# Optimization experiments

Measured on AMD Instinct MI355X. Metric: run time of the kernel, lower is better.

Reference implementation:

```python
import jax, jax.numpy as jnp
import numpy as np

H = 1024      # controller hidden size
M = 4096      # memory rows (must equal WORD per original code's buffer shapes)
WORD = 4096   # word size
R = 4         # read heads
NW = 2        # write heads
MODES = 1 + 2 * NW
EPS = 1e-3


def _lin(x, W, b):
    return x @ W.T + b


def _allocation(usage):
    # usage: [1, M] -> allocation weighting via ascending usage sort (DNC)
    u = EPS + (1.0 - EPS) * usage
    order = jnp.argsort(u, axis=1)                       # ascending (least used first)
    sorted_u = jnp.take_along_axis(u, order, axis=1)
    prod = jnp.cumprod(sorted_u, axis=1)
    excl = jnp.concatenate([jnp.ones((1, 1), u.dtype), prod[:, :-1]], axis=1)
    sorted_alloc = (1.0 - sorted_u) * excl
    return jnp.zeros_like(u).at[0, order[0]].set(sorted_alloc[0])


def _dnc_forward(x, memory, prev_read_weights, prev_write_weights, prev_link,
                 prev_precedence, prev_usage,
                 W_wv, b_wv, W_ev, b_ev, W_fg, b_fg, W_ag, b_ag, W_wg, b_wg,
                 W_rm, b_rm, W_wk, b_wk, W_ws, b_ws, W_rk, b_rk, W_rs, b_rs):
    # ---- read_inputs ----
    write_vector = _lin(x, W_wv, b_wv).reshape(NW, WORD)
    erase_vector = jax.nn.sigmoid(_lin(x, W_ev, b_ev)).reshape(NW, WORD)
    free_gate = jax.nn.sigmoid(_lin(x, W_fg, b_fg))          # [1,R]
    allocation_gate = jax.nn.sigmoid(_lin(x, W_ag, b_ag))    # [1,NW]
    write_gate = jax.nn.sigmoid(_lin(x, W_wg, b_wg))         # [1,NW]
    read_mode = jax.nn.sigmoid(_lin(x, W_rm, b_rm)).reshape(R, MODES)
    write_keys = jax.nn.sigmoid(_lin(x, W_wk, b_wk)).reshape(NW, WORD)
    write_strengths = _lin(x, W_ws, b_ws)                    # [1,NW]
    read_keys = _lin(x, W_rk, b_rk).reshape(R, WORD)
    read_strengths = _lin(x, W_rs, b_rs)                     # [1,R]

    # ---- usage ----
    ww_term = 1.0 - jnp.prod(prev_write_weights, axis=1)                   # [1,M]
    usage = prev_usage + (1.0 - prev_usage) * ww_term
    phi = 1.0 - jnp.prod(free_gate[..., None] * prev_read_weights, axis=1)
    usage = usage * phi

    # ---- write weights (cosine content + sequential allocation per head) ----
    dot = jnp.einsum('wd,bmd->bwm', write_keys, memory)                    # [1,NW,M]
    mem_norms = jnp.sqrt(jnp.sum(memory * memory, axis=2))                 # [1,M]
    key_norms = jnp.sqrt(jnp.sum(write_keys * write_keys, axis=1))         # [NW]
    similarity = dot / (key_norms[None, :, None] * mem_norms[:, None, :] + EPS)

    write_gates = (allocation_gate * write_gate)[..., None]                # [1,NW,1]
    ww_rows = []
    for i in range(NW):  # small fixed head loop (sequential usage dependency)
        beta = 1.0 + jax.nn.softplus(write_strengths[0, i])
        cw = jax.nn.softmax(similarity[0, i] * beta)                       # [M]
        a = _allocation(usage)                                             # [1,M]
        usage = usage + (1.0 - usage) * write_gates[:, i, :] * a
        ww_rows.append(write_gate[0, i] * (allocation_gate[0, i] * a[0]
                       + (1.0 - allocation_gate[0, i]) * cw))
    write_weights = jnp.stack(ww_rows)[None]                               # [1,NW,M]

    # ---- erase and write ----
    weighted_resets = write_weights[..., None] * erase_vector[None, :, None, :]
    reset_gate = jnp.prod(1.0 - weighted_resets, axis=1)                   # [1,M,WORD]
    new_memory = memory * reset_gate + jnp.einsum('bwm,wd->bmd', write_weights, write_vector)

    # ---- temporal linkage ----
    wi = write_weights[..., None]          # [1,NW,M,1]
    wj = write_weights[:, :, None, :]      # [1,NW,1,M]
    pj = prev_precedence[:, :, None, :]    # [1,NW,1,M]
    link = (1.0 - wi - wj) * prev_link + wi * pj
    link = link * (1.0 - jnp.eye(M, dtype=link.dtype))
    write_sum = jnp.sum(write_weights, axis=2, keepdims=True)
    precedence = (1.0 - write_sum) * prev_precedence + write_weights

    # ---- read weights ----
    rdot = jnp.einsum('rd,bmd->brm', read_keys, new_memory)
    new_mem_norms = jnp.sqrt(jnp.sum(new_memory * new_memory, axis=2))
    rkey_norms = jnp.sqrt(jnp.sum(read_keys * read_keys, axis=1))
    rsim = rdot / (rkey_norms[None, :, None] * new_mem_norms[:, None, :])  # note: no eps here (as in source)
    content_weights = jax.nn.softmax(rsim * read_strengths[0][None, :, None], axis=-1)

    expanded = jnp.broadcast_to(prev_read_weights[:, None], (1, NW, R, M))  # stack((rw,rw)) with NW=2
    fwd_w = jnp.einsum('bwrm,bwnm->brwn', expanded, link)   # rw @ link^T, permuted -> [1,R,NW,M]
    bwd_w = jnp.einsum('bwrm,bwmn->brwn', expanded, link)   # rw @ link,   permuted -> [1,R,NW,M]
    rm = read_mode[None]                                    # [1,R,MODES]
    backward_mode = rm[:, :, :NW]
    forward_mode = rm[:, :, NW:2 * NW]
    content_mode = rm[:, :, 2 * NW:]                        # [1,R,1]
    read_weights = (jnp.einsum('brw,brwm->brm', backward_mode, bwd_w)
                    + jnp.einsum('brw,brwm->brm', forward_mode, fwd_w)
                    + content_mode * content_weights)
    read_words = jnp.einsum('brm,bmd->brd', read_weights, new_memory)      # [1,R,WORD]
    return read_words, new_memory, read_weights, write_weights, link, precedence, usage


def setup_inputs() -> dict:
    key = jax.random.key(0)
    ks = jax.random.split(key, 32)
    rn = lambda i, s: jax.random.normal(ks[i], s, dtype=jnp.float32)
    ru = lambda i, s: jax.random.uniform(ks[i], s, dtype=jnp.float32)
    w = lambda i, s: rn(i, s) * 0.02
    return {
        'x': rn(0, (1, H)),
        'memory': rn(1, (1, M, WORD)),
        'prev_read_weights': ru(2, (1, R, M)),
        'prev_write_weights': ru(3, (1, NW, M)),
        'prev_link': ru(4, (1, NW, M, M)),
        'prev_precedence': ru(5, (1, NW, M)),
        'prev_usage': ru(6, (1, M)),
        'W_wv': w(7, (NW * WORD, H)), 'b_wv': jnp.zeros((NW * WORD,), jnp.float32),
        'W_ev': w(8, (NW * WORD, H)), 'b_ev': jnp.zeros((NW * WORD,), jnp.float32),
        'W_fg': w(9, (R, H)), 'b_fg': jnp.zeros((R,), jnp.float32),
        'W_ag': w(10, (NW, H)), 'b_ag': jnp.zeros((NW,), jnp.float32),
        'W_wg': w(11, (NW, H)), 'b_wg': jnp.zeros((NW,), jnp.float32),
        'W_rm': w(12, (R * MODES, H)), 'b_rm': jnp.zeros((R * MODES,), jnp.float32),
        'W_wk': w(13, (NW * WORD, H)), 'b_wk': jnp.zeros((NW * WORD,), jnp.float32),
        'W_ws': w(14, (NW, H)), 'b_ws': jnp.zeros((NW,), jnp.float32),
        'W_rk': w(15, (R * WORD, H)), 'b_rk': jnp.zeros((R * WORD,), jnp.float32),
        'W_rs': w(16, (R, H)), 'b_rs': jnp.zeros((R,), jnp.float32),
    }


def reference(x, memory, prev_read_weights, prev_write_weights, prev_link,
              prev_precedence, prev_usage,
              W_wv, b_wv, W_ev, b_ev, W_fg, b_fg, W_ag, b_ag, W_wg, b_wg,
              W_rm, b_rm, W_wk, b_wk, W_ws, b_ws, W_rk, b_rk, W_rs, b_rs):
    return _dnc_forward(x, memory, prev_read_weights, prev_write_weights, prev_link,
                        prev_precedence, prev_usage,
                        W_wv, b_wv, W_ev, b_ev, W_fg, b_fg, W_ag, b_ag, W_wg, b_wg,
                        W_rm, b_rm, W_wk, b_wk, W_ws, b_ws, W_rk, b_rk, W_rs, b_rs)
```

## Files before the change

### kernel.cpp

```cpp
#include <hip/hip_runtime.h>
#include <math.h>

#define HD 1024
#define MD 4096
#define WD 4096
#define RD 4
#define NWD 2
#define MODESD 5
#define EPSF 0.001f

#define O_WORDS 0
#define O_NM    16384
#define O_RW    16793600
#define O_WW    16809984
#define O_LINK  16818176
#define O_PREC  50372608
#define O_USAGE 50380800

#define WS_WV   0
#define WS_EV   8192
#define WS_WK   16384
#define WS_RK   24576
#define WS_FG   40960
#define WS_AG   40976
#define WS_WG   40992
#define WS_RM   41008
#define WS_WSTR 41040
#define WS_RS   41056
#define WS_KN   41072
#define WS_RKN  41088
#define WS_UPRE 41104
#define WS_SIM  45200
#define WS_RDOT 53392
#define WS_NMN  69776
#define WS_CONT 73872
#define WS_FWD  90256
#define WS_CW   123024
#define WS_UU   131216
#define WS_LU   135312
#define WS_S0   139408
#define WS_S1   143504
#define WS_WWSUM 147600
#define WS_BWD  147604
#define WS_ZERO_START WS_S0
#define WS_ZERO_COUNT (4096 + 4096 + 4 + 32768)

__device__ __forceinline__ float waveReduceSum(float v) {
#pragma unroll
  for (int o = 32; o; o >>= 1) v += __shfl_down(v, o, 64);
  return v;
}

__global__ void gemv_kernel(const float* __restrict__ W, const float* __restrict__ b,
                            const float* __restrict__ x, float* __restrict__ out,
                            int rows, int act) {
  __shared__ float4 xs[HD / 4];
  int t = threadIdx.x;
  const float4* x4 = (const float4*)x;
  xs[t] = x4[t];
  __syncthreads();
  int wave = t >> 6, lane = t & 63;
  int row = blockIdx.x * 4 + wave;
  if (row >= rows) return;
  const float4* W4 = (const float4*)(W + (size_t)row * HD);
  float acc = 0.f;
#pragma unroll
  for (int i = 0; i < 4; ++i) {
    float4 w = W4[i * 64 + lane];
    float4 xv = xs[i * 64 + lane];
    acc += w.x * xv.x + w.y * xv.y + w.z * xv.z + w.w * xv.w;
  }
  acc = waveReduceSum(acc);
  if (lane == 0) {
    float v = acc + b[row];
    if (act) v = 1.f / (1.f + expf(-v));
    out[row] = v;
  }
}

__global__ void small_gemv_kernel(const float* __restrict__ x,
                                  const float* __restrict__ Wfg, const float* __restrict__ bfg,
                                  const float* __restrict__ Wag, const float* __restrict__ bag,
                                  const float* __restrict__ Wwg, const float* __restrict__ bwg,
                                  const float* __restrict__ Wrm, const float* __restrict__ brm,
                                  const float* __restrict__ Wws, const float* __restrict__ bws,
                                  const float* __restrict__ Wrs, const float* __restrict__ brs,
                                  float* __restrict__ ws) {
  int blk = blockIdx.x;
  const float* W; const float* b; float* out; int row; int act;
  if (blk < 4)       { W = Wfg; b = bfg; out = ws + WS_FG;   row = blk;       act = 1; }
  else if (blk < 6)  { W = Wag; b = bag; out = ws + WS_AG;   row = blk - 4;   act = 1; }
  else if (blk < 8)  { W = Wwg; b = bwg; out = ws + WS_WG;   row = blk - 6;   act = 1; }
  else if (blk < 28) { W = Wrm; b = brm; out = ws + WS_RM;   row = blk - 8;   act = 1; }
  else if (blk < 30) { W = Wws; b = bws; out = ws + WS_WSTR; row = blk - 28;  act = 0; }
  else               { W = Wrs; b = brs; out = ws + WS_RS;   row = blk - 30;  act = 0; }
  int t = threadIdx.x;
  const float4* W4 = (const float4*)(W + (size_t)row * HD);
  const float4* x4 = (const float4*)x;
  float4 w = W4[t], xv = x4[t];
  float acc = w.x * xv.x + w.y * xv.y + w.z * xv.z + w.w * xv.w;
  acc = waveReduceSum(acc);
  __shared__ float sh[4];
  int wave = t >> 6, lane = t & 63;
  if (lane == 0) sh[wave] = acc;
  __syncthreads();
  if (t == 0) {
    float v = sh[0] + sh[1] + sh[2] + sh[3] + b[row];
    if (act) v = 1.f / (1.f + expf(-v));
    out[row] = v;
  }
}

__global__ void norms_kernel(const float* __restrict__ wk, const float* __restrict__ rk,
                             float* __restrict__ kn, float* __restrict__ rkn) {
  int v = blockIdx.x;
  const float* p = (v < 2) ? (wk + v * WD) : (rk + (v - 2) * WD);
  float s = 0.f;
  for (int d = threadIdx.x; d < WD; d += 256) { float t = p[d]; s += t * t; }
  s = waveReduceSum(s);
  __shared__ float sh[4];
  int wave = threadIdx.x >> 6, lane = threadIdx.x & 63;
  if (lane == 0) sh[wave] = s;
  __syncthreads();
  if (threadIdx.x == 0) {
    float r = sqrtf(sh[0] + sh[1] + sh[2] + sh[3]);
    if (v < 2) kn[v] = r; else rkn[v - 2] = r;
  }
}

__global__ void usage_kernel(const float* __restrict__ pusage, const float* __restrict__ pww,
                             const float* __restrict__ prw, const float* __restrict__ fg,
                             float* __restrict__ upre, float* __restrict__ uu,
                             float* __restrict__ lu) {
  int m = blockIdx.x * 256 + threadIdx.x;
  float pw = 1.f;
#pragma unroll
  for (int w = 0; w < NWD; ++w) pw *= pww[w * MD + m];
  float pu = pusage[m];
  float u = pu + (1.f - pu) * (1.f - pw);
  float pr = 1.f;
#pragma unroll
  for (int r = 0; r < RD; ++r) pr *= fg[r] * prw[r * MD + m];
  float up = u * (1.f - pr);
  upre[m] = up;
  float v = EPSF + (1.f - EPSF) * up;
  uu[m] = v;
  lu[m] = logf(v);
}

__global__ void sim_kernel(const float* __restrict__ mem, const float* __restrict__ wk,
                           const float* __restrict__ kn, float* __restrict__ sim) {
  int m = blockIdx.x;
  int t = threadIdx.x;
  const float4* row = (const float4*)(mem + (size_t)m * WD);
  const float4* k0 = (const float4*)wk;
  const float4* k1 = (const float4*)(wk + WD);
  float d0 = 0, d1 = 0, s = 0;
  for (int i = t; i < WD / 4; i += 256) {
    float4 v = row[i], a = k0[i], b = k1[i];
    d0 += v.x * a.x + v.y * a.y + v.z * a.z + v.w * a.w;
    d1 += v.x * b.x + v.y * b.y + v.z * b.z + v.w * b.w;
    s  += v.x * v.x + v.y * v.y + v.z * v.z + v.w * v.w;
  }
  d0 = waveReduceSum(d0); d1 = waveReduceSum(d1); s = waveReduceSum(s);
  __shared__ float sh[3][4];
  int wave = t >> 6, lane = t & 63;
  if (lane == 0) { sh[0][wave] = d0; sh[1][wave] = d1; sh[2][wave] = s; }
  __syncthreads();
  if (t == 0) {
    float D0 = sh[0][0] + sh[0][1] + sh[0][2] + sh[0][3];
    float D1 = sh[1][0] + sh[1][1] + sh[1][2] + sh[1][3];
    float S  = sh[2][0] + sh[2][1] + sh[2][2] + sh[2][3];
    float mn = sqrtf(S);
    sim[0 * MD + m] = D0 / (kn[0] * mn + EPSF);
    sim[1 * MD + m] = D1 / (kn[1] * mn + EPSF);
  }
}

__global__ void cw_kernel(const float* __restrict__ sim, const float* __restrict__ wstr,
                          float* __restrict__ cw) {
  int h = blockIdx.x;
  int t = threadIdx.x;
  __shared__ float vals[MD];
  __shared__ float red[256];
  float beta = 1.f + log1pf(expf(wstr[h]));
  float mx = -3.4e38f;
  for (int m = t; m < MD; m += 256) {
    float v = sim[h * MD + m] * beta;
    vals[m] = v; mx = fmaxf(mx, v);
  }
  red[t] = mx; __syncthreads();
  for (int s = 128; s; s >>= 1) { if (t < s) red[t] = fmaxf(red[t], red[t + s]); __syncthreads(); }
  mx = red[0]; __syncthreads();
  float sm = 0.f;
  for (int m = t; m < MD; m += 256) { float e = expf(vals[m] - mx); vals[m] = e; sm += e; }
  red[t] = sm; __syncthreads();
  for (int s = 128; s; s >>= 1) { if (t < s) red[t] += red[t + s]; __syncthreads(); }
  float inv = 1.f / red[0];
  for (int m = t; m < MD; m += 256) cw[h * MD + m] = vals[m] * inv;
}

__global__ void alloc_partial_kernel(const float* __restrict__ uu, const float* __restrict__ lu,
                                     float* __restrict__ S) {
  __shared__ float4 us[64], ls[64];
  int t = threadIdx.x;
  int j0 = blockIdx.y * 256;
  if (t < 64) {
    us[t] = ((const float4*)(uu + j0))[t];
    ls[t] = ((const float4*)(lu + j0))[t];
  }
  __syncthreads();
  int i = blockIdx.x * 256 + t;
  float ui = uu[i];
  float s = 0.f;
#pragma unroll 4
  for (int c = 0; c < 64; ++c) {
    float4 u4 = us[c], l4 = ls[c];
    int jb = j0 + c * 4;
    s += ((u4.x < ui) || (u4.x == ui && (jb + 0) < i)) ? l4.x : 0.f;
    s += ((u4.y < ui) || (u4.y == ui && (jb + 1) < i)) ? l4.y : 0.f;
    s += ((u4.z < ui) || (u4.z == ui && (jb + 2) < i)) ? l4.z : 0.f;
    s += ((u4.w < ui) || (u4.w == ui && (jb + 3) < i)) ? l4.w : 0.f;
  }
  atomicAdd(&S[i], s);
}

__global__ void update0_kernel(const float* __restrict__ S0, const float* __restrict__ cw,
                               const float* __restrict__ ag, const float* __restrict__ wg,
                               const float* __restrict__ upre, float* __restrict__ uu,
                               float* __restrict__ lu, float* __restrict__ u1,
                               float* __restrict__ out_ww, float* __restrict__ wwsum) {
  int m = blockIdx.x * 256 + threadIdx.x;
  float agv = ag[0], wgv = wg[0];
  float uum = uu[m];
  float a = (1.f - uum) * expf(S0[m]);
  float w = wgv * (agv * a + (1.f - agv) * cw[m]);
  out_ww[m] = w;
  float up = upre[m];
  float un = up + (1.f - up) * (agv * wgv) * a;
  u1[m] = un;
  float v = EPSF + (1.f - EPSF) * un;
  uu[m] = v;
  lu[m] = logf(v);
  float p = waveReduceSum(w);
  if ((threadIdx.x & 63) == 0) atomicAdd(&wwsum[0], p);
}

__global__ void update1_kernel(const float* __restrict__ S1, const float* __restrict__ cw,
                               const float* __restrict__ ag, const float* __restrict__ wg,
                               const float* __restrict__ u1, const float* __restrict__ uu,
                               float* __restrict__ out_ww, float* __restrict__ out_usage,
                               float* __restrict__ wwsum) {
  int m = blockIdx.x * 256 + threadIdx.x;
  float agv = ag[1], wgv = wg[1];
  float uum = uu[m];
  float a = (1.f - uum) * expf(S1[m]);
  float w = wgv * (agv * a + (1.f - agv) * cw[MD + m]);
  out_ww[MD + m] = w;
  float un = u1[m];
  out_usage[m] = un + (1.f - un) * (agv * wgv) * a;
  float p = waveReduceSum(w);
  if ((threadIdx.x & 63) == 0) atomicAdd(&wwsum[1], p);
}

__global__ void prec_kernel(const float* __restrict__ ww, const float* __restrict__ wwsum,
                            const float* __restrict__ pprec, float* __restrict__ out_prec) {
  int m = blockIdx.x * 256 + threadIdx.x;
  float s0 = wwsum[0], s1 = wwsum[1];
  out_prec[m] = (1.f - s0) * pprec[m] + ww[m];
  out_prec[MD + m] = (1.f - s1) * pprec[MD + m] + ww[MD + m];
}

__global__ void newmem_kernel(const float* __restrict__ mem, const float* __restrict__ ww,
                              const float* __restrict__ ev, const float* __restrict__ wvv,
                              const float* __restrict__ rk, float* __restrict__ nm_out,
                              float* __restrict__ rdot, float* __restrict__ nmn) {
  int m = blockIdx.x;
  int t = threadIdx.x;
  float w0 = ww[m], w1 = ww[MD + m];
  const float4* row = (const float4*)(mem + (size_t)m * WD);
  const float4* e0 = (const float4*)ev;
  const float4* e1 = (const float4*)(ev + WD);
  const float4* v0 = (const float4*)wvv;
  const float4* v1 = (const float4*)(wvv + WD);
  const float4* k0 = (const float4*)rk;
  const float4* k1 = (const float4*)(rk + WD);
  const float4* k2 = (const float4*)(rk + 2 * WD);
  const float4* k3 = (const float4*)(rk + 3 * WD);
  float4* outp = (float4*)(nm_out + (size_t)m * WD);
  float r0 = 0, r1 = 0, r2 = 0, r3 = 0, s2 = 0;
  for (int i = t; i < WD / 4; i += 256) {
    float4 mv = row[i], ea = e0[i], eb = e1[i], va = v0[i], vb = v1[i];
    float4 o;
    o.x = mv.x * (1.f - w0 * ea.x) * (1.f - w1 * eb.x) + w0 * va.x + w1 * vb.x;
    o.y = mv.y * (1.f - w0 * ea.y) * (1.f - w1 * eb.y) + w0 * va.y + w1 * vb.y;
    o.z = mv.z * (1.f - w0 * ea.z) * (1.f - w1 * eb.z) + w0 * va.z + w1 * vb.z;
    o.w = mv.w * (1.f - w0 * ea.w) * (1.f - w1 * eb.w) + w0 * va.w + w1 * vb.w;
    outp[i] = o;
    float4 a = k0[i]; r0 += o.x * a.x + o.y * a.y + o.z * a.z + o.w * a.w;
    float4 b = k1[i]; r1 += o.x * b.x + o.y * b.y + o.z * b.z + o.w * b.w;
    float4 c = k2[i]; r2 += o.x * c.x + o.y * c.y + o.z * c.z + o.w * c.w;
    float4 d = k3[i]; r3 += o.x * d.x + o.y * d.y + o.z * d.z + o.w * d.w;
    s2 += o.x * o.x + o.y * o.y + o.z * o.z + o.w * o.w;
  }
  r0 = waveReduceSum(r0); r1 = waveReduceSum(r1); r2 = waveReduceSum(r2);
  r3 = waveReduceSum(r3); s2 = waveReduceSum(s2);
  __shared__ float sh[5][4];
  int wave = t >> 6, lane = t & 63;
  if (lane == 0) { sh[0][wave] = r0; sh[1][wave] = r1; sh[2][wave] = r2; sh[3][wave] = r3; sh[4][wave] = s2; }
  __syncthreads();
  if (t == 0) {
    rdot[0 * MD + m] = sh[0][0] + sh[0][1] + sh[0][2] + sh[0][3];
    rdot[1 * MD + m] = sh[1][0] + sh[1][1] + sh[1][2] + sh[1][3];
    rdot[2 * MD + m] = sh[2][0] + sh[2][1] + sh[2][2] + sh[2][3];
    rdot[3 * MD + m] = sh[3][0] + sh[3][1] + sh[3][2] + sh[3][3];
    nmn[m] = sqrtf(sh[4][0] + sh[4][1] + sh[4][2] + sh[4][3]);
  }
}

__global__ void content_kernel(const float* __restrict__ rdot, const float* __restrict__ nmn,
                               const float* __restrict__ rkn, const float* __restrict__ rs,
                               float* __restrict__ cont) {
  int r = blockIdx.x;
  int t = threadIdx.x;
  __shared__ float vals[MD];
  __shared__ float red[256];
  float strength = rs[r], kn = rkn[r];
  float mx = -3.4e38f;
  for (int m = t; m < MD; m += 256) {
    float v = rdot[r * MD + m] / (kn * nmn[m]) * strength;
    vals[m] = v; mx = fmaxf(mx, v);
  }
  red[t] = mx; __syncthreads();
  for (int s = 128; s; s >>= 1) { if (t < s) red[t] = fmaxf(red[t], red[t + s]); __syncthreads(); }
  mx = red[0]; __syncthreads();
  float sm = 0.f;
  for (int m = t; m < MD; m += 256) { float e = expf(vals[m] - mx); vals[m] = e; sm += e; }
  red[t] = sm; __syncthreads();
  for (int s = 128; s; s >>= 1) { if (t < s) red[t] += red[t + s]; __syncthreads(); }
  float inv = 1.f / red[0];
  for (int m = t; m < MD; m += 256) cont[r * MD + m] = vals[m] * inv;
}

__global__ void link_kernel(const float* __restrict__ plink, const float* __restrict__ ww,
                            const float* __restrict__ pprec, const float* __restrict__ prw,
                            float* __restrict__ link_out, float* __restrict__ fwd) {
  int i = blockIdx.x;
  int w = blockIdx.y;
  int t = threadIdx.x;
  float wwi = ww[w * MD + i];
  const float4* pl = (const float4*)(plink + ((size_t)w * MD + i) * MD);
  const float4* wj = (const float4*)(ww + w * MD);
  const float4* pj = (const float4*)(pprec + w * MD);
  const float4* p0 = (const float4*)prw;
  const float4* p1 = (const float4*)(prw + MD);
  const float4* p2 = (const float4*)(prw + 2 * MD);
  const float4* p3 = (const float4*)(prw + 3 * MD);
  float4* lo = (float4*)(link_out + ((size_t)w * MD + i) * MD);
  float f0 = 0, f1 = 0, f2 = 0, f3 = 0;
  for (int c = t; c < MD / 4; c += 256) {
    float4 L = pl[c], WJ = wj[c], PJ = pj[c];
    float4 o;
    o.x = (1.f - wwi - WJ.x) * L.x + wwi * PJ.x;
    o.y = (1.f - wwi - WJ.y) * L.y + wwi * PJ.y;
    o.z = (1.f - wwi - WJ.z) * L.z + wwi * PJ.z;
    o.w = (1.f - wwi - WJ.w) * L.w + wwi * PJ.w;
    int j0 = c * 4;
    if ((unsigned)(i - j0) < 4u) ((float*)&o)[i - j0] = 0.f;
    lo[c] = o;
    float4 a = p0[c]; f0 += o.x * a.x + o.y * a.y + o.z * a.z + o.w * a.w;
    float4 b = p1[c]; f1 += o.x * b.x + o.y * b.y + o.z * b.z + o.w * b.w;
    float4 cc = p2[c]; f2 += o.x * cc.x + o.y * cc.y + o.z * cc.z + o.w * cc.w;
    float4 d = p3[c]; f3 += o.x * d.x + o.y * d.y + o.z * d.z + o.w * d.w;
  }
  f0 = waveReduceSum(f0); f1 = waveReduceSum(f1);
  f2 = waveReduceSum(f2); f3 = waveReduceSum(f3);
  __shared__ float sh[4][4];
  int wave = t >> 6, lane = t & 63;
  if (lane == 0) { sh[0][wave] = f0; sh[1][wave] = f1; sh[2][wave] = f2; sh[3][wave] = f3; }
  __syncthreads();
  if (t == 0) {
    fwd[(0 * NWD + w) * MD + i] = sh[0][0] + sh[0][1] + sh[0][2] + sh[0][3];
    fwd[(1 * NWD + w) * MD + i] = sh[1][0] + sh[1][1] + sh[1][2] + sh[1][3];
    fwd[(2 * NWD + w) * MD + i] = sh[2][0] + sh[2][1] + sh[2][2] + sh[2][3];
    fwd[(3 * NWD + w) * MD + i] = sh[3][0] + sh[3][1] + sh[3][2] + sh[3][3];
  }
}

__global__ void bwd_kernel(const float* __restrict__ link, const float* __restrict__ prw,
                           float* __restrict__ bwd) {
  int mc = blockIdx.x, jt = blockIdx.y, w = blockIdx.z;
  int j = jt * 256 + threadIdx.x;
  const float* base = link + (size_t)w * MD * MD;
  float a0 = 0, a1 = 0, a2 = 0, a3 = 0;
  int m0 = mc * 256;
  for (int m = m0; m < m0 + 256; ++m) {
    float lv = base[(size_t)m * MD + j];
    a0 += prw[m] * lv;
    a1 += prw[MD + m] * lv;
    a2 += prw[2 * MD + m] * lv;
    a3 += prw[3 * MD + m] * lv;
  }
  atomicAdd(&bwd[(0 * NWD + w) * MD + j], a0);
  atomicAdd(&bwd[(1 * NWD + w) * MD + j], a1);
  atomicAdd(&bwd[(2 * NWD + w) * MD + j], a2);
  atomicAdd(&bwd[(3 * NWD + w) * MD + j], a3);
}

__global__ void rw_kernel(const float* __restrict__ fwd, const float* __restrict__ bwd,
                          const float* __restrict__ cont, const float* __restrict__ rm,
                          float* __restrict__ out_rw) {
  int idx = blockIdx.x * 256 + threadIdx.x;
  int r = idx >> 12;
  int m = idx & (MD - 1);
  float v = rm[r * MODESD + 4] * cont[idx];
#pragma unroll
  for (int w = 0; w < NWD; ++w) {
    v += rm[r * MODESD + w] * bwd[(r * NWD + w) * MD + m];
    v += rm[r * MODESD + NWD + w] * fwd[(r * NWD + w) * MD + m];
  }
  out_rw[idx] = v;
}

__global__ void rwords_kernel(const float* __restrict__ rw, const float* __restrict__ nm,
                              float* __restrict__ out_words) {
  int mc = blockIdx.x;
  int d = blockIdx.y * 256 + threadIdx.x;
  float a0 = 0, a1 = 0, a2 = 0, a3 = 0;
  int m0 = mc * 256;
  for (int m = m0; m < m0 + 256; ++m) {
    float v = nm[(size_t)m * WD + d];
    a0 += rw[m] * v;
    a1 += rw[MD + m] * v;
    a2 += rw[2 * MD + m] * v;
    a3 += rw[3 * MD + m] * v;
  }
  atomicAdd(&out_words[d], a0);
  atomicAdd(&out_words[WD + d], a1);
  atomicAdd(&out_words[2 * WD + d], a2);
  atomicAdd(&out_words[3 * WD + d], a3);
}

extern "C" void kernel_launch(void* const* d_in, const int* in_sizes, int n_in,
                              void* d_out, int out_size, void* d_ws, size_t ws_size,
                              hipStream_t stream) {
  (void)in_sizes; (void)n_in; (void)out_size; (void)ws_size;
  const float* x      = (const float*)d_in[0];
  const float* memory = (const float*)d_in[1];
  const float* prw    = (const float*)d_in[2];
  const float* pww    = (const float*)d_in[3];
  const float* plink  = (const float*)d_in[4];
  const float* pprec  = (const float*)d_in[5];
  const float* pusage = (const float*)d_in[6];
  float* ws  = (float*)d_ws;
  float* out = (float*)d_out;

  hipMemsetAsync(ws + WS_ZERO_START, 0, WS_ZERO_COUNT * sizeof(float), stream);
  hipMemsetAsync(out + O_WORDS, 0, 16384 * sizeof(float), stream);

  gemv_kernel<<<2048, 256, 0, stream>>>((const float*)d_in[7],  (const float*)d_in[8],  x, ws + WS_WV, 8192, 0);
  gemv_kernel<<<2048, 256, 0, stream>>>((const float*)d_in[9],  (const float*)d_in[10], x, ws + WS_EV, 8192, 1);
  gemv_kernel<<<2048, 256, 0, stream>>>((const float*)d_in[19], (const float*)d_in[20], x, ws + WS_WK, 8192, 1);
  gemv_kernel<<<4096, 256, 0, stream>>>((const float*)d_in[23], (const float*)d_in[24], x, ws + WS_RK, 16384, 0);
  small_gemv_kernel<<<34, 256, 0, stream>>>(x,
      (const float*)d_in[11], (const float*)d_in[12],
      (const float*)d_in[13], (const float*)d_in[14],
      (const float*)d_in[15], (const float*)d_in[16],
      (const float*)d_in[17], (const float*)d_in[18],
      (const float*)d_in[21], (const float*)d_in[22],
      (const float*)d_in[25], (const float*)d_in[26],
      ws);

  norms_kernel<<<6, 256, 0, stream>>>(ws + WS_WK, ws + WS_RK, ws + WS_KN, ws + WS_RKN);
  usage_kernel<<<16, 256, 0, stream>>>(pusage, pww, prw, ws + WS_FG, ws + WS_UPRE, ws + WS_UU, ws + WS_LU);
  sim_kernel<<<4096, 256, 0, stream>>>(memory, ws + WS_WK, ws + WS_KN, ws + WS_SIM);
  cw_kernel<<<2, 256, 0, stream>>>(ws + WS_SIM, ws + WS_WSTR, ws + WS_CW);

  alloc_partial_kernel<<<dim3(16, 16), 256, 0, stream>>>(ws + WS_UU, ws + WS_LU, ws + WS_S0);
  update0_kernel<<<16, 256, 0, stream>>>(ws + WS_S0, ws + WS_CW, ws + WS_AG, ws + WS_WG,
                                         ws + WS_UPRE, ws + WS_UU, ws + WS_LU, ws + WS_UPRE,
                                         out + O_WW, ws + WS_WWSUM);
  alloc_partial_kernel<<<dim3(16, 16), 256, 0, stream>>>(ws + WS_UU, ws + WS_LU, ws + WS_S1);
  update1_kernel<<<16, 256, 0, stream>>>(ws + WS_S1, ws + WS_CW, ws + WS_AG, ws + WS_WG,
                                         ws + WS_UPRE, ws + WS_UU, out + O_WW, out + O_USAGE,
                                         ws + WS_WWSUM);
  prec_kernel<<<16, 256, 0, stream>>>(out + O_WW, ws + WS_WWSUM, pprec, out + O_PREC);

  newmem_kernel<<<4096, 256, 0, stream>>>(memory, out + O_WW, ws + WS_EV, ws + WS_WV,
                                          ws + WS_RK, out + O_NM, ws + WS_RDOT, ws + WS_NMN);
  content_kernel<<<4, 256, 0, stream>>>(ws + WS_RDOT, ws + WS_NMN, ws + WS_RKN, ws + WS_RS, ws + WS_CONT);
  link_kernel<<<dim3(MD, NWD), 256, 0, stream>>>(plink, out + O_WW, pprec, prw,
                                                 out + O_LINK, ws + WS_FWD);
  bwd_kernel<<<dim3(16, 16, 2), 256, 0, stream>>>(out + O_LINK, prw, ws + WS_BWD);
  rw_kernel<<<64, 256, 0, stream>>>(ws + WS_FWD, ws + WS_BWD, ws + WS_CONT, ws + WS_RM, out + O_RW);
  rwords_kernel<<<dim3(16, 16), 256, 0, stream>>>(out + O_RW, out + O_NM, out + O_WORDS);
}
```

Before: 684.7 us.

## Fuse GEMVs, alloc chain with grid barrier, and link forward/backward passes

Merges all controller GEMVs into one launch with nontemporal weight loads, folds the key norms into the sim and content kernels, and collapses the usage/allocation/update/precedence sequence into one 64-block kernel synchronised by a software grid barrier. The link update is tiled so that a single pass over the two 64MB link matrices computes the new link (written with nontemporal stores) together with the forward and backward products, instead of rereading the link in a separate backward kernel. The grid barrier assumes all 64 blocks are resident at once, and atomics now accumulate forward and backward partials.

```diff
diff --git a/kernel.cpp b/kernel.cpp
--- a/kernel.cpp
+++ b/kernel.cpp
@@ -27,23 +27,34 @@
 #define WS_RM   41008
 #define WS_WSTR 41040
 #define WS_RS   41056
-#define WS_KN   41072
-#define WS_RKN  41088
 #define WS_UPRE 41104
 #define WS_SIM  45200
 #define WS_RDOT 53392
 #define WS_NMN  69776
 #define WS_CONT 73872
-#define WS_FWD  90256
 #define WS_CW   123024
 #define WS_UU   131216
 #define WS_LU   135312
-#define WS_S0   139408
-#define WS_S1   143504
+#define WS_S0    139408
+#define WS_S1    143504
 #define WS_WWSUM 147600
-#define WS_BWD  147604
+#define WS_BAR   147604
+#define WS_FWD   147620
+#define WS_BWD   180388
 #define WS_ZERO_START WS_S0
-#define WS_ZERO_COUNT (4096 + 4096 + 4 + 32768)
+#define WS_ZERO_COUNT (213156 - 139408)
+
+typedef float floatx4 __attribute__((ext_vector_type(4)));
+
+__device__ __forceinline__ float4 ntload4(const float4* p) {
+  floatx4 t = __builtin_nontemporal_load((const floatx4*)p);
+  float4 r; r.x = t.x; r.y = t.y; r.z = t.z; r.w = t.w;
+  return r;
+}
+__device__ __forceinline__ void ntstore4(float4* p, float4 v) {
+  floatx4 t; t.x = v.x; t.y = v.y; t.z = v.z; t.w = v.w;
+  __builtin_nontemporal_store(t, (floatx4*)p);
+}
 
 __device__ __forceinline__ float waveReduceSum(float v) {
 #pragma unroll
@@ -51,129 +62,84 @@
   return v;
 }
 
-__global__ void gemv_kernel(const float* __restrict__ W, const float* __restrict__ b,
-                            const float* __restrict__ x, float* __restrict__ out,
-                            int rows, int act) {
+__global__ void __launch_bounds__(256) gemv_all_kernel(
+    const float* __restrict__ x,
+    const float* __restrict__ Wwv, const float* __restrict__ bwv,
+    const float* __restrict__ Wev, const float* __restrict__ bev,
+    const float* __restrict__ Wwk, const float* __restrict__ bwk,
+    const float* __restrict__ Wrk, const float* __restrict__ brk,
+    const float* __restrict__ Wfg, const float* __restrict__ bfg,
+    const float* __restrict__ Wag, const float* __restrict__ bag,
+    const float* __restrict__ Wwg, const float* __restrict__ bwg,
+    const float* __restrict__ Wrm, const float* __restrict__ brm,
+    const float* __restrict__ Wws, const float* __restrict__ bws,
+    const float* __restrict__ Wrs, const float* __restrict__ brs,
+    float* __restrict__ ws) {
   __shared__ float4 xs[HD / 4];
   int t = threadIdx.x;
-  const float4* x4 = (const float4*)x;
-  xs[t] = x4[t];
+  xs[t] = ((const float4*)x)[t];
   __syncthreads();
   int wave = t >> 6, lane = t & 63;
   int row = blockIdx.x * 4 + wave;
-  if (row >= rows) return;
-  const float4* W4 = (const float4*)(W + (size_t)row * HD);
+  if (row >= 40994) return;
+  const float* W; const float* b; float* out; int r; int act;
+  if (row < 8192)       { W = Wwv; b = bwv; out = ws + WS_WV;   r = row;         act = 0; }
+  else if (row < 16384) { W = Wev; b = bev; out = ws + WS_EV;   r = row - 8192;  act = 1; }
+  else if (row < 24576) { W = Wwk; b = bwk; out = ws + WS_WK;   r = row - 16384; act = 1; }
+  else if (row < 40960) { W = Wrk; b = brk; out = ws + WS_RK;   r = row - 24576; act = 0; }
+  else if (row < 40964) { W = Wfg; b = bfg; out = ws + WS_FG;   r = row - 40960; act = 1; }
+  else if (row < 40966) { W = Wag; b = bag; out = ws + WS_AG;   r = row - 40964; act = 1; }
+  else if (row < 40968) { W = Wwg; b = bwg; out = ws + WS_WG;   r = row - 40966; act = 1; }
+  else if (row < 40988) { W = Wrm; b = brm; out = ws + WS_RM;   r = row - 40968; act = 1; }
+  else if (row < 40990) { W = Wws; b = bws; out = ws + WS_WSTR; r = row - 40988; act = 0; }
+  else                  { W = Wrs; b = brs; out = ws + WS_RS;   r = row - 40990; act = 0; }
+  const float4* W4 = (const float4*)(W + (size_t)r * HD);
   float acc = 0.f;
 #pragma unroll
   for (int i = 0; i < 4; ++i) {
-    float4 w = W4[i * 64 + lane];
+    float4 w = ntload4(W4 + i * 64 + lane);
     float4 xv = xs[i * 64 + lane];
     acc += w.x * xv.x + w.y * xv.y + w.z * xv.z + w.w * xv.w;
   }
   acc = waveReduceSum(acc);
   if (lane == 0) {
-    float v = acc + b[row];
+    float v = acc + b[r];
     if (act) v = 1.f / (1.f + expf(-v));
-    out[row] = v;
-  }
-}
-
-__global__ void small_gemv_kernel(const float* __restrict__ x,
-                                  const float* __restrict__ Wfg, const float* __restrict__ bfg,
-                                  const float* __restrict__ Wag, const float* __restrict__ bag,
-                                  const float* __restrict__ Wwg, const float* __restrict__ bwg,
-                                  const float* __restrict__ Wrm, const float* __restrict__ brm,
-                                  const float* __restrict__ Wws, const float* __restrict__ bws,
-                                  const float* __restrict__ Wrs, const float* __restrict__ brs,
-                                  float* __restrict__ ws) {
-  int blk = blockIdx.x;
-  const float* W; const float* b; float* out; int row; int act;
-  if (blk < 4)       { W = Wfg; b = bfg; out = ws + WS_FG;   row = blk;       act = 1; }
-  else if (blk < 6)  { W = Wag; b = bag; out = ws + WS_AG;   row = blk - 4;   act = 1; }
-  else if (blk < 8)  { W = Wwg; b = bwg; out = ws + WS_WG;   row = blk - 6;   act = 1; }
-  else if (blk < 28) { W = Wrm; b = brm; out = ws + WS_RM;   row = blk - 8;   act = 1; }
-  else if (blk < 30) { W = Wws; b = bws; out = ws + WS_WSTR; row = blk - 28;  act = 0; }
-  else               { W = Wrs; b = brs; out = ws + WS_RS;   row = blk - 30;  act = 0; }
-  int t = threadIdx.x;
-  const float4* W4 = (const float4*)(W + (size_t)row * HD);
-  const float4* x4 = (const float4*)x;
-  float4 w = W4[t], xv = x4[t];
-  float acc = w.x * xv.x + w.y * xv.y + w.z * xv.z + w.w * xv.w;
-  acc = waveReduceSum(acc);
-  __shared__ float sh[4];
-  int wave = t >> 6, lane = t & 63;
-  if (lane == 0) sh[wave] = acc;
-  __syncthreads();
-  if (t == 0) {
-    float v = sh[0] + sh[1] + sh[2] + sh[3] + b[row];
-    if (act) v = 1.f / (1.f + expf(-v));
-    out[row] = v;
-  }
-}
-
-__global__ void norms_kernel(const float* __restrict__ wk, const float* __restrict__ rk,
-                             float* __restrict__ kn, float* __restrict__ rkn) {
-  int v = blockIdx.x;
-  const float* p = (v < 2) ? (wk + v * WD) : (rk + (v - 2) * WD);
-  float s = 0.f;
-  for (int d = threadIdx.x; d < WD; d += 256) { float t = p[d]; s += t * t; }
-  s = waveReduceSum(s);
-  __shared__ float sh[4];
-  int wave = threadIdx.x >> 6, lane = threadIdx.x & 63;
-  if (lane == 0) sh[wave] = s;
-  __syncthreads();
-  if (threadIdx.x == 0) {
-    float r = sqrtf(sh[0] + sh[1] + sh[2] + sh[3]);
-    if (v < 2) kn[v] = r; else rkn[v - 2] = r;
-  }
-}
-
-__global__ void usage_kernel(const float* __restrict__ pusage, const float* __restrict__ pww,
-                             const float* __restrict__ prw, const float* __restrict__ fg,
-                             float* __restrict__ upre, float* __restrict__ uu,
-                             float* __restrict__ lu) {
-  int m = blockIdx.x * 256 + threadIdx.x;
-  float pw = 1.f;
-#pragma unroll
-  for (int w = 0; w < NWD; ++w) pw *= pww[w * MD + m];
-  float pu = pusage[m];
-  float u = pu + (1.f - pu) * (1.f - pw);
-  float pr = 1.f;
-#pragma unroll
-  for (int r = 0; r < RD; ++r) pr *= fg[r] * prw[r * MD + m];
-  float up = u * (1.f - pr);
-  upre[m] = up;
-  float v = EPSF + (1.f - EPSF) * up;
-  uu[m] = v;
-  lu[m] = logf(v);
+    out[r] = v;
+  }
 }
 
 __global__ void sim_kernel(const float* __restrict__ mem, const float* __restrict__ wk,
-                           const float* __restrict__ kn, float* __restrict__ sim) {
+                           float* __restrict__ sim) {
   int m = blockIdx.x;
   int t = threadIdx.x;
   const float4* row = (const float4*)(mem + (size_t)m * WD);
   const float4* k0 = (const float4*)wk;
   const float4* k1 = (const float4*)(wk + WD);
-  float d0 = 0, d1 = 0, s = 0;
+  float d0 = 0, d1 = 0, s = 0, n0 = 0, n1 = 0;
   for (int i = t; i < WD / 4; i += 256) {
     float4 v = row[i], a = k0[i], b = k1[i];
     d0 += v.x * a.x + v.y * a.y + v.z * a.z + v.w * a.w;
     d1 += v.x * b.x + v.y * b.y + v.z * b.z + v.w * b.w;
     s  += v.x * v.x + v.y * v.y + v.z * v.z + v.w * v.w;
+    n0 += a.x * a.x + a.y * a.y + a.z * a.z + a.w * a.w;
+    n1 += b.x * b.x + b.y * b.y + b.z * b.z + b.w * b.w;
   }
   d0 = waveReduceSum(d0); d1 = waveReduceSum(d1); s = waveReduceSum(s);
-  __shared__ float sh[3][4];
+  n0 = waveReduceSum(n0); n1 = waveReduceSum(n1);
+  __shared__ float sh[5][4];
   int wave = t >> 6, lane = t & 63;
-  if (lane == 0) { sh[0][wave] = d0; sh[1][wave] = d1; sh[2][wave] = s; }
+  if (lane == 0) { sh[0][wave] = d0; sh[1][wave] = d1; sh[2][wave] = s; sh[3][wave] = n0; sh[4][wave] = n1; }
   __syncthreads();
   if (t == 0) {
     float D0 = sh[0][0] + sh[0][1] + sh[0][2] + sh[0][3];
     float D1 = sh[1][0] + sh[1][1] + sh[1][2] + sh[1][3];
     float S  = sh[2][0] + sh[2][1] + sh[2][2] + sh[2][3];
+    float N0 = sh[3][0] + sh[3][1] + sh[3][2] + sh[3][3];
+    float N1 = sh[4][0] + sh[4][1] + sh[4][2] + sh[4][3];
     float mn = sqrtf(S);
-    sim[0 * MD + m] = D0 / (kn[0] * mn + EPSF);
-    sim[1 * MD + m] = D1 / (kn[1] * mn + EPSF);
+    sim[0 * MD + m] = D0 / (sqrtf(N0) * mn + EPSF);
+    sim[1 * MD + m] = D1 / (sqrtf(N1) * mn + EPSF);
   }
 }
 
@@ -200,75 +166,125 @@
   for (int m = t; m < MD; m += 256) cw[h * MD + m] = vals[m] * inv;
 }
 
-__global__ void alloc_partial_kernel(const float* __restrict__ uu, const float* __restrict__ lu,
-                                     float* __restrict__ S) {
-  __shared__ float4 us[64], ls[64];
-  int t = threadIdx.x;
-  int j0 = blockIdx.y * 256;
-  if (t < 64) {
-    us[t] = ((const float4*)(uu + j0))[t];
-    ls[t] = ((const float4*)(lu + j0))[t];
-  }
-  __syncthreads();
-  int i = blockIdx.x * 256 + t;
-  float ui = uu[i];
-  float s = 0.f;
+#define AB 64
+
+__device__ __forceinline__ void gridbar(unsigned* c, int id) {
+  __syncthreads();
+  if (threadIdx.x == 0) {
+    __threadfence();
+    atomicAdd(&c[id], 1u);
+    while (atomicAdd(&c[id], 0u) < AB) __builtin_amdgcn_s_sleep(8);
+  }
+  __syncthreads();
+  __threadfence();
+}
+
+__global__ void __launch_bounds__(256)
+alloc_chain_kernel(const float* __restrict__ pusage, const float* __restrict__ pww,
+                   const float* __restrict__ prw, const float* __restrict__ pprec,
+                   float* __restrict__ ws, float* __restrict__ out_ww,
+                   float* __restrict__ out_usage, float* __restrict__ out_prec) {
+  float* upre = ws + WS_UPRE;
+  float* uu = ws + WS_UU;
+  float* lu = ws + WS_LU;
+  float* S0 = ws + WS_S0;
+  float* S1 = ws + WS_S1;
+  float* wwsum = ws + WS_WWSUM;
+  const float* cw = ws + WS_CW;
+  const float* fg = ws + WS_FG;
+  const float* ag = ws + WS_AG;
+  const float* wg = ws + WS_WG;
+  unsigned* bar = (unsigned*)(ws + WS_BAR);
+  int tid = threadIdx.x;
+  int idx = blockIdx.x * 256 + tid;
+  __shared__ float lds_u[1024], lds_l[1024];
+
+  if (idx < MD) {
+    float pw = pww[idx] * pww[MD + idx];
+    float pu = pusage[idx];
+    float u = pu + (1.f - pu) * (1.f - pw);
+    float pr = 1.f;
+#pragma unroll
+    for (int r = 0; r < RD; ++r) pr *= fg[r] * prw[r * MD + idx];
+    float up = u * (1.f - pr);
+    upre[idx] = up;
+    float v = EPSF + (1.f - EPSF) * up;
+    uu[idx] = v;
+    lu[idx] = logf(v);
+  }
+  gridbar(bar, 0);
+
+  {
+    int jq = blockIdx.x >> 4;
+    int i = ((blockIdx.x & 15) << 8) + tid;
+    int j0 = jq << 10;
+    for (int k = tid; k < 1024; k += 256) { lds_u[k] = uu[j0 + k]; lds_l[k] = lu[j0 + k]; }
+    __syncthreads();
+    float ui = uu[i];
+    float s = 0.f;
 #pragma unroll 4
-  for (int c = 0; c < 64; ++c) {
-    float4 u4 = us[c], l4 = ls[c];
-    int jb = j0 + c * 4;
-    s += ((u4.x < ui) || (u4.x == ui && (jb + 0) < i)) ? l4.x : 0.f;
-    s += ((u4.y < ui) || (u4.y == ui && (jb + 1) < i)) ? l4.y : 0.f;
-    s += ((u4.z < ui) || (u4.z == ui && (jb + 2) < i)) ? l4.z : 0.f;
-    s += ((u4.w < ui) || (u4.w == ui && (jb + 3) < i)) ? l4.w : 0.f;
-  }
-  atomicAdd(&S[i], s);
-}
-
-__global__ void update0_kernel(const float* __restrict__ S0, const float* __restrict__ cw,
-                               const float* __restrict__ ag, const float* __restrict__ wg,
-                               const float* __restrict__ upre, float* __restrict__ uu,
-                               float* __restrict__ lu, float* __restrict__ u1,
-                               float* __restrict__ out_ww, float* __restrict__ wwsum) {
-  int m = blockIdx.x * 256 + threadIdx.x;
-  float agv = ag[0], wgv = wg[0];
-  float uum = uu[m];
-  float a = (1.f - uum) * expf(S0[m]);
-  float w = wgv * (agv * a + (1.f - agv) * cw[m]);
-  out_ww[m] = w;
-  float up = upre[m];
-  float un = up + (1.f - up) * (agv * wgv) * a;
-  u1[m] = un;
-  float v = EPSF + (1.f - EPSF) * un;
-  uu[m] = v;
-  lu[m] = logf(v);
-  float p = waveReduceSum(w);
-  if ((threadIdx.x & 63) == 0) atomicAdd(&wwsum[0], p);
-}
-
-__global__ void update1_kernel(const float* __restrict__ S1, const float* __restrict__ cw,
-                               const float* __restrict__ ag, const float* __restrict__ wg,
-                               const float* __restrict__ u1, const float* __restrict__ uu,
-                               float* __restrict__ out_ww, float* __restrict__ out_usage,
-                               float* __restrict__ wwsum) {
-  int m = blockIdx.x * 256 + threadIdx.x;
-  float agv = ag[1], wgv = wg[1];
-  float uum = uu[m];
-  float a = (1.f - uum) * expf(S1[m]);
-  float w = wgv * (agv * a + (1.f - agv) * cw[MD + m]);
-  out_ww[MD + m] = w;
-  float un = u1[m];
-  out_usage[m] = un + (1.f - un) * (agv * wgv) * a;
-  float p = waveReduceSum(w);
-  if ((threadIdx.x & 63) == 0) atomicAdd(&wwsum[1], p);
-}
-
-__global__ void prec_kernel(const float* __restrict__ ww, const float* __restrict__ wwsum,
-                            const float* __restrict__ pprec, float* __restrict__ out_prec) {
-  int m = blockIdx.x * 256 + threadIdx.x;
-  float s0 = wwsum[0], s1 = wwsum[1];
-  out_prec[m] = (1.f - s0) * pprec[m] + ww[m];
-  out_prec[MD + m] = (1.f - s1) * pprec[MD + m] + ww[MD + m];
+    for (int k = 0; k < 1024; ++k) {
+      int j = j0 + k;
+      float uj = lds_u[k];
+      s += ((uj < ui) || (uj == ui && j < i)) ? lds_l[k] : 0.f;
+    }
+    atomicAdd(&S0[i], s);
+  }
+  gridbar(bar, 1);
+
+  if (idx < MD) {
+    float agv = ag[0], wgv = wg[0];
+    float uum = uu[idx];
+    float a = (1.f - uum) * expf(S0[idx]);
+    float w = wgv * (agv * a + (1.f - agv) * cw[idx]);
+    out_ww[idx] = w;
+    float up = upre[idx];
+    float un = up + (1.f - up) * (agv * wgv) * a;
+    upre[idx] = un;
+    float v = EPSF + (1.f - EPSF) * un;
+    uu[idx] = v;
+    lu[idx] = logf(v);
+    float p = waveReduceSum(w);
+    if ((tid & 63) == 0) atomicAdd(&wwsum[0], p);
+  }
+  gridbar(bar, 2);
+
+  {
+    int jq = blockIdx.x >> 4;
+    int i = ((blockIdx.x & 15) << 8) + tid;
+    int j0 = jq << 10;
+    for (int k = tid; k < 1024; k += 256) { lds_u[k] = uu[j0 + k]; lds_l[k] = lu[j0 + k]; }
+    __syncthreads();
+    float ui = uu[i];
+    float s = 0.f;
+#pragma unroll 4
+    for (int k = 0; k < 1024; ++k) {
+      int j = j0 + k;
+      float uj = lds_u[k];
+      s += ((uj < ui) || (uj == ui && j < i)) ? lds_l[k] : 0.f;
+    }
+    atomicAdd(&S1[i], s);
+  }
+  gridbar(bar, 3);
+
+  if (idx < MD) {
+    float agv = ag[1], wgv = wg[1];
+    float uum = uu[idx];
+    float a = (1.f - uum) * expf(S1[idx]);
+    float w = wgv * (agv * a + (1.f - agv) * cw[MD + idx]);
+    out_ww[MD + idx] = w;
+    float un = upre[idx];
+    out_usage[idx] = un + (1.f - un) * (agv * wgv) * a;
+    float p = waveReduceSum(w);
+    if ((tid & 63) == 0) atomicAdd(&wwsum[1], p);
+  }
+  gridbar(bar, 4);
+
+  if (idx < MD) {
+    float s0 = wwsum[0], s1 = wwsum[1];
+    out_prec[idx] = (1.f - s0) * pprec[idx] + out_ww[idx];
+    out_prec[MD + idx] = (1.f - s1) * pprec[MD + idx] + out_ww[MD + idx];
+  }
 }
 
 __global__ void newmem_kernel(const float* __restrict__ mem, const float* __restrict__ ww,
@@ -319,13 +335,19 @@
 }
 
 __global__ void content_kernel(const float* __restrict__ rdot, const float* __restrict__ nmn,
-                               const float* __restrict__ rkn, const float* __restrict__ rs,
+                               const float* __restrict__ rk, const float* __restrict__ rs,
                                float* __restrict__ cont) {
   int r = blockIdx.x;
   int t = threadIdx.x;
   __shared__ float vals[MD];
   __shared__ float red[256];
-  float strength = rs[r], kn = rkn[r];
+  const float* kr = rk + (size_t)r * WD;
+  float s2 = 0.f;
+  for (int d = t; d < WD; d += 256) { float v = kr[d]; s2 += v * v; }
+  red[t] = s2; __syncthreads();
+  for (int s = 128; s; s >>= 1) { if (t < s) red[t] += red[t + s]; __syncthreads(); }
+  float kn = sqrtf(red[0]); __syncthreads();
+  float strength = rs[r];
   float mx = -3.4e38f;
   for (int m = t; m < MD; m += 256) {
     float v = rdot[r * MD + m] / (kn * nmn[m]) * strength;
@@ -342,69 +364,88 @@
   for (int m = t; m < MD; m += 256) cont[r * MD + m] = vals[m] * inv;
 }
 
-__global__ void link_kernel(const float* __restrict__ plink, const float* __restrict__ ww,
-                            const float* __restrict__ pprec, const float* __restrict__ prw,
-                            float* __restrict__ link_out, float* __restrict__ fwd) {
-  int i = blockIdx.x;
-  int w = blockIdx.y;
-  int t = threadIdx.x;
-  float wwi = ww[w * MD + i];
-  const float4* pl = (const float4*)(plink + ((size_t)w * MD + i) * MD);
-  const float4* wj = (const float4*)(ww + w * MD);
-  const float4* pj = (const float4*)(pprec + w * MD);
-  const float4* p0 = (const float4*)prw;
-  const float4* p1 = (const float4*)(prw + MD);
-  const float4* p2 = (const float4*)(prw + 2 * MD);
-  const float4* p3 = (const float4*)(prw + 3 * MD);
-  float4* lo = (float4*)(link_out + ((size_t)w * MD + i) * MD);
-  float f0 = 0, f1 = 0, f2 = 0, f3 = 0;
-  for (int c = t; c < MD / 4; c += 256) {
-    float4 L = pl[c], WJ = wj[c], PJ = pj[c];
+#define LMT 64
+__global__ void __launch_bounds__(256) link_fused_kernel(
+    const float* __restrict__ plink, const float* __restrict__ ww,
+    const float* __restrict__ pprec, const float* __restrict__ prw,
+    float* __restrict__ link_out, float* __restrict__ fwd, float* __restrict__ bwd) {
+  int mc = blockIdx.x, jc = blockIdx.y, w = blockIdx.z;
+  int tid = threadIdx.x;
+  __shared__ float ww_s[LMT];
+  __shared__ float prw_s[4][LMT];
+  __shared__ float fwd_s[LMT][4];
+  int m0 = mc * LMT;
+  for (int k = tid; k < LMT; k += 256) {
+    ww_s[k] = ww[w * MD + m0 + k];
+    prw_s[0][k] = prw[0 * MD + m0 + k];
+    prw_s[1][k] = prw[1 * MD + m0 + k];
+    prw_s[2][k] = prw[2 * MD + m0 + k];
+    prw_s[3][k] = prw[3 * MD + m0 + k];
+  }
+  for (int k = tid; k < LMT * 4; k += 256) ((float*)fwd_s)[k] = 0.f;
+  __syncthreads();
+  int j0 = jc * 1024 + tid * 4;
+  float4 wwj = *(const float4*)(ww + w * MD + j0);
+  float4 pj  = *(const float4*)(pprec + w * MD + j0);
+  float4 q0  = *(const float4*)(prw + 0 * MD + j0);
+  float4 q1  = *(const float4*)(prw + 1 * MD + j0);
+  float4 q2  = *(const float4*)(prw + 2 * MD + j0);
+  float4 q3  = *(const float4*)(prw + 3 * MD + j0);
+  float4 a0 = make_float4(0.f, 0.f, 0.f, 0.f), a1 = a0, a2 = a0, a3 = a0;
+  int lane = tid & 63;
+  const size_t base = (size_t)w * MD * MD;
+#pragma unroll 2
+  for (int mi = 0; mi < LMT; ++mi) {
+    int mg = m0 + mi;
+    float wwi = ww_s[mi];
+    float4 L = ntload4((const float4*)(plink + base + (size_t)mg * MD + j0));
     float4 o;
-    o.x = (1.f - wwi - WJ.x) * L.x + wwi * PJ.x;
-    o.y = (1.f - wwi - WJ.y) * L.y + wwi * PJ.y;
-    o.z = (1.f - wwi - WJ.z) * L.z + wwi * PJ.z;
-    o.w = (1.f - wwi - WJ.w) * L.w + wwi * PJ.w;
-    int j0 = c * 4;
-    if ((unsigned)(i - j0) < 4u) ((float*)&o)[i - j0] = 0.f;
-    lo[c] = o;
-    float4 a = p0[c]; f0 += o.x * a.x + o.y * a.y + o.z * a.z + o.w * a.w;
-    float4 b = p1[c]; f1 += o.x * b.x + o.y * b.y + o.z * b.z + o.w * b.w;
-    float4 cc = p2[c]; f2 += o.x * cc.x + o.y * cc.y + o.z * cc.z + o.w * cc.w;
-    float4 d = p3[c]; f3 += o.x * d.x + o.y * d.y + o.z * d.z + o.w * d.w;
-  }
-  f0 = waveReduceSum(f0); f1 = waveReduceSum(f1);
-  f2 = waveReduceSum(f2); f3 = waveReduceSum(f3);
-  __shared__ float sh[4][4];
-  int wave = t >> 6, lane = t & 63;
-  if (lane == 0) { sh[0][wave] = f0; sh[1][wave] = f1; sh[2][wave] = f2; sh[3][wave] = f3; }
-  __syncthreads();
-  if (t == 0) {
-    fwd[(0 * NWD + w) * MD + i] = sh[0][0] + sh[0][1] + sh[0][2] + sh[0][3];
-    fwd[(1 * NWD + w) * MD + i] = sh[1][0] + sh[1][1] + sh[1][2] + sh[1][3];
-    fwd[(2 * NWD + w) * MD + i] = sh[2][0] + sh[2][1] + sh[2][2] + sh[2][3];
-    fwd[(3 * NWD + w) * MD + i] = sh[3][0] + sh[3][1] + sh[3][2] + sh[3][3];
-  }
-}
-
-__global__ void bwd_kernel(const float* __restrict__ link, const float* __restrict__ prw,
-                           float* __restrict__ bwd) {
-  int mc = blockIdx.x, jt = blockIdx.y, w = blockIdx.z;
-  int j = jt * 256 + threadIdx.x;
-  const float* base = link + (size_t)w * MD * MD;
-  float a0 = 0, a1 = 0, a2 = 0, a3 = 0;
-  int m0 = mc * 256;
-  for (int m = m0; m < m0 + 256; ++m) {
-    float lv = base[(size_t)m * MD + j];
-    a0 += prw[m] * lv;
-    a1 += prw[MD + m] * lv;
-    a2 += prw[2 * MD + m] * lv;
-    a3 += prw[3 * MD + m] * lv;
-  }
-  atomicAdd(&bwd[(0 * NWD + w) * MD + j], a0);
-  atomicAdd(&bwd[(1 * NWD + w) * MD + j], a1);
-  atomicAdd(&bwd[(2 * NWD + w) * MD + j], a2);
-  atomicAdd(&bwd[(3 * NWD + w) * MD + j], a3);
+    o.x = (1.f - wwi - wwj.x) * L.x + wwi * pj.x;
+    o.y = (1.f - wwi - wwj.y) * L.y + wwi * pj.y;
+    o.z = (1.f - wwi - wwj.z) * L.z + wwi * pj.z;
+    o.w = (1.f - wwi - wwj.w) * L.w + wwi * pj.w;
+    int dj = mg - j0;
+    o.x = (dj == 0) ? 0.f : o.x;
+    o.y = (dj == 1) ? 0.f : o.y;
+    o.z = (dj == 2) ? 0.f : o.z;
+    o.w = (dj == 3) ? 0.f : o.w;
+    ntstore4((float4*)(link_out + base + (size_t)mg * MD + j0), o);
+    float pm0 = prw_s[0][mi], pm1 = prw_s[1][mi], pm2 = prw_s[2][mi], pm3 = prw_s[3][mi];
+    a0.x += pm0 * o.x; a0.y += pm0 * o.y; a0.z += pm0 * o.z; a0.w += pm0 * o.w;
+    a1.x += pm1 * o.x; a1.y += pm1 * o.y; a1.z += pm1 * o.z; a1.w += pm1 * o.w;
+    a2.x += pm2 * o.x; a2.y += pm2 * o.y; a2.z += pm2 * o.z; a2.w += pm2 * o.w;
+    a3.x += pm3 * o.x; a3.y += pm3 * o.y; a3.z += pm3 * o.z; a3.w += pm3 * o.w;
+    float s0 = o.x * q0.x + o.y * q0.y + o.z * q0.z + o.w * q0.w;
+    float s1 = o.x * q1.x + o.y * q1.y + o.z * q1.z + o.w * q1.w;
+    float s2 = o.x * q2.x + o.y * q2.y + o.z * q2.z + o.w * q2.w;
+    float s3 = o.x * q3.x + o.y * q3.y + o.z * q3.z + o.w * q3.w;
+#pragma unroll
+    for (int off = 32; off; off >>= 1) {
+      s0 += __shfl_down(s0, off, 64);
+      s1 += __shfl_down(s1, off, 64);
+      s2 += __shfl_down(s2, off, 64);
+      s3 += __shfl_down(s3, off, 64);
+    }
+    if (lane == 0) {
+      atomicAdd(&fwd_s[mi][0], s0);
+      atomicAdd(&fwd_s[mi][1], s1);
+      atomicAdd(&fwd_s[mi][2], s2);
+      atomicAdd(&fwd_s[mi][3], s3);
+    }
+  }
+  __syncthreads();
+  for (int k = tid; k < LMT * 4; k += 256) {
+    int mi = k >> 2, r = k & 3;
+    atomicAdd(&fwd[(r * NWD + w) * MD + m0 + mi], fwd_s[mi][r]);
+  }
+  float* b0 = bwd + (size_t)(0 * NWD + w) * MD + j0;
+  float* b1 = bwd + (size_t)(1 * NWD + w) * MD + j0;
+  float* b2 = bwd + (size_t)(2 * NWD + w) * MD + j0;
+  float* b3 = bwd + (size_t)(3 * NWD + w) * MD + j0;
+  atomicAdd(b0 + 0, a0.x); atomicAdd(b0 + 1, a0.y); atomicAdd(b0 + 2, a0.z); atomicAdd(b0 + 3, a0.w);
+  atomicAdd(b1 + 0, a1.x); atomicAdd(b1 + 1, a1.y); atomicAdd(b1 + 2, a1.z); atomicAdd(b1 + 3, a1.w);
+  atomicAdd(b2 + 0, a2.x); atomicAdd(b2 + 1, a2.y); atomicAdd(b2 + 2, a2.z); atomicAdd(b2 + 3, a2.w);
+  atomicAdd(b3 + 0, a3.x); atomicAdd(b3 + 1, a3.y); atomicAdd(b3 + 2, a3.z); atomicAdd(b3 + 3, a3.w);
 }
 
 __global__ void rw_kernel(const float* __restrict__ fwd, const float* __restrict__ bwd,
@@ -458,11 +499,11 @@
   hipMemsetAsync(ws + WS_ZERO_START, 0, WS_ZERO_COUNT * sizeof(float), stream);
   hipMemsetAsync(out + O_WORDS, 0, 16384 * sizeof(float), stream);
 
-  gemv_kernel<<<2048, 256, 0, stream>>>((const float*)d_in[7],  (const float*)d_in[8],  x, ws + WS_WV, 8192, 0);
-  gemv_kernel<<<2048, 256, 0, stream>>>((const float*)d_in[9],  (const float*)d_in[10], x, ws + WS_EV, 8192, 1);
-  gemv_kernel<<<2048, 256, 0, stream>>>((const float*)d_in[19], (const float*)d_in[20], x, ws + WS_WK, 8192, 1);
-  gemv_kernel<<<4096, 256, 0, stream>>>((const float*)d_in[23], (const float*)d_in[24], x, ws + WS_RK, 16384, 0);
-  small_gemv_kernel<<<34, 256, 0, stream>>>(x,
+  gemv_all_kernel<<<10249, 256, 0, stream>>>(x,
+      (const float*)d_in[7],  (const float*)d_in[8],
+      (const float*)d_in[9],  (const float*)d_in[10],
+      (const float*)d_in[19], (const float*)d_in[20],
+      (const float*)d_in[23], (const float*)d_in[24],
       (const float*)d_in[11], (const float*)d_in[12],
       (const float*)d_in[13], (const float*)d_in[14],
       (const float*)d_in[15], (const float*)d_in[16],
@@ -471,27 +512,18 @@
       (const float*)d_in[25], (const float*)d_in[26],
       ws);
 
-  norms_kernel<<<6, 256, 0, stream>>>(ws + WS_WK, ws + WS_RK, ws + WS_KN, ws + WS_RKN);
-  usage_kernel<<<16, 256, 0, stream>>>(pusage, pww, prw, ws + WS_FG, ws + WS_UPRE, ws + WS_UU, ws + WS_LU);
-  sim_kernel<<<4096, 256, 0, stream>>>(memory, ws + WS_WK, ws + WS_KN, ws + WS_SIM);
+  sim_kernel<<<4096, 256, 0, stream>>>(memory, ws + WS_WK, ws + WS_SIM);
   cw_kernel<<<2, 256, 0, stream>>>(ws + WS_SIM, ws + WS_WSTR, ws + WS_CW);
 
-  alloc_partial_kernel<<<dim3(16, 16), 256, 0, stream>>>(ws + WS_UU, ws + WS_LU, ws + WS_S0);
-  update0_kernel<<<16, 256, 0, stream>>>(ws + WS_S0, ws + WS_CW, ws + WS_AG, ws + WS_WG,
-                                         ws + WS_UPRE, ws + WS_UU, ws + WS_LU, ws + WS_UPRE,
-                                         out + O_WW, ws + WS_WWSUM);
-  alloc_partial_kernel<<<dim3(16, 16), 256, 0, stream>>>(ws + WS_UU, ws + WS_LU, ws + WS_S1);
-  update1_kernel<<<16, 256, 0, stream>>>(ws + WS_S1, ws + WS_CW, ws + WS_AG, ws + WS_WG,
-                                         ws + WS_UPRE, ws + WS_UU, out + O_WW, out + O_USAGE,
-                                         ws + WS_WWSUM);
-  prec_kernel<<<16, 256, 0, stream>>>(out + O_WW, ws + WS_WWSUM, pprec, out + O_PREC);
+  alloc_chain_kernel<<<AB, 256, 0, stream>>>(pusage, pww, prw, pprec, ws,
+                                             out + O_WW, out + O_USAGE, out + O_PREC);
 
   newmem_kernel<<<4096, 256, 0, stream>>>(memory, out + O_WW, ws + WS_EV, ws + WS_WV,
                                           ws + WS_RK, out + O_NM, ws + WS_RDOT, ws + WS_NMN);
-  content_kernel<<<4, 256, 0, stream>>>(ws + WS_RDOT, ws + WS_NMN, ws + WS_RKN, ws + WS_RS, ws + WS_CONT);
-  link_kernel<<<dim3(MD, NWD), 256, 0, stream>>>(plink, out + O_WW, pprec, prw,
-                                                 out + O_LINK, ws + WS_FWD);
-  bwd_kernel<<<dim3(16, 16, 2), 256, 0, stream>>>(out + O_LINK, prw, ws + WS_BWD);
+  content_kernel<<<4, 256, 0, stream>>>(ws + WS_RDOT, ws + WS_NMN, ws + WS_RK, ws + WS_RS, ws + WS_CONT);
+
+  link_fused_kernel<<<dim3(64, 4, 2), 256, 0, stream>>>(plink, out + O_WW, pprec, prw,
+                                                        out + O_LINK, ws + WS_FWD, ws + WS_BWD);
   rw_kernel<<<64, 256, 0, stream>>>(ws + WS_FWD, ws + WS_BWD, ws + WS_CONT, ws + WS_RM, out + O_RW);
   rwords_kernel<<<dim3(16, 16), 256, 0, stream>>>(out + O_RW, out + O_NM, out + O_WORDS);
 }
```

Result: slower. 802.5 us (+17.2%).
